# Kernel tuning notes

Measured on AMD Instinct MI355X. Metric: run time of the kernel, lower is better.

## Reference

```python
import jax, jax.numpy as jnp
import numpy as np

B, T, I, H, NL, O = 256, 512, 64, 256, 2, 4


def _lstm_layer(x, Wih, Whh, bih, bhh):
    # x: [B, T, I_in]; Wih: [4H, I_in]; Whh: [4H, H]; biases: [4H]
    # PyTorch gate order: i, f, g, o
    xg = jnp.einsum('bti,gi->btg', x, Wih) + (bih + bhh)  # [B, T, 4H]
    h0 = jnp.zeros((x.shape[0], Whh.shape[1]), x.dtype)
    c0 = jnp.zeros_like(h0)

    def step(carry, xg_t):
        h, c = carry
        g = xg_t + h @ Whh.T
        i, f, gg, o = jnp.split(g, 4, axis=-1)
        c = jax.nn.sigmoid(f) * c + jax.nn.sigmoid(i) * jnp.tanh(gg)
        h = jax.nn.sigmoid(o) * jnp.tanh(c)
        return (h, c), h

    (_, _), hs = jax.lax.scan(step, (h0, c0), jnp.swapaxes(xg, 0, 1))  # [T, B, H]
    return jnp.swapaxes(hs, 0, 1)  # [B, T, H]


def setup_inputs() -> dict:
    key = jax.random.key(0)
    ks = jax.random.split(key, 16)
    s = 1.0 / np.sqrt(H)
    u = lambda k, shape: jax.random.uniform(k, shape, jnp.float32, -s, s)
    return {
        'x': jax.random.normal(ks[0], (B, T, I), jnp.float32),
        'Wih0': u(ks[1], (4 * H, I)),
        'Whh0': u(ks[2], (4 * H, H)),
        'bih0': u(ks[3], (4 * H,)),
        'bhh0': u(ks[4], (4 * H,)),
        'Wih1': u(ks[5], (4 * H, H)),
        'Whh1': u(ks[6], (4 * H, H)),
        'bih1': u(ks[7], (4 * H,)),
        'bhh1': u(ks[8], (4 * H,)),
        'W1': u(ks[9], (5 * H, H)),
        'b1': u(ks[10], (5 * H,)),
        'W2': u(ks[11], (O, 5 * H)),
        'b2': u(ks[12], (O,)),
    }


def reference(x, Wih0, Whh0, bih0, bhh0, Wih1, Whh1, bih1, bhh1, W1, b1, W2, b2):
    h1 = _lstm_layer(x, Wih0, Whh0, bih0, bhh0)   # [B, T, H]
    h2 = _lstm_layer(h1, Wih1, Whh1, bih1, bhh1)  # [B, T, H]
    last = h2[:, -1, :]                            # [B, H]
    y = last @ W1.T + b1                           # [B, 5H]
    y = y @ W2.T + b2                              # [B, O]
    return y
```

## Files before the change

kernel.cpp:

```cpp
#include <hip/hip_runtime.h>
#include <stdint.h>

typedef unsigned short u16;
typedef unsigned int   u32;
typedef unsigned long long u64;
typedef __bf16 bf16_t;
typedef bf16_t bf16x8 __attribute__((ext_vector_type(8)));
typedef float  f32x4  __attribute__((ext_vector_type(4)));
typedef int    i32x4  __attribute__((ext_vector_type(4)));

#define NSTEPS 512
#define SPIN_LIM  (1<<17)
#define RETRY_LIM (1<<13)

#define WS_RING1 0u
#define WS_RING2 1048576u
#define WS_PROG  2097152u
#define WS_TOTAL 2098176u

#define SMEM_BYTES (64*520*2)

__device__ __forceinline__ u16 f2bf(float f) {
  u32 u = __float_as_uint(f);
  return (u16)((u + 0x7fffu + ((u >> 16) & 1u)) >> 16);
}
__device__ __forceinline__ float bf2f(u16 b) { return __uint_as_float(((u32)b) << 16); }
__device__ __forceinline__ float sigf(float x) { return 1.f / (1.f + __expf(-x)); }
__device__ __forceinline__ float tanhf_(float x) {
  float e = __expf(-2.f * fabsf(x));
  float t = (1.f - e) / (1.f + e);
  return x >= 0.f ? t : -t;
}

__device__ __forceinline__ void pub_u32(u32* p, u32 v) {
  (void)__hip_atomic_exchange(p, v, __ATOMIC_RELAXED, __HIP_MEMORY_SCOPE_AGENT);
}
__device__ __forceinline__ u64 ld_u64_sc1(const u64* p) {
  u64 v; asm volatile("global_load_dwordx2 %0, %1, off sc1\n\ts_waitcnt vmcnt(0)"
                      : "=v"(v) : "v"(p) : "memory"); return v;
}

#define LD16_W(A, P)                                                       \
  asm volatile(                                                            \
    "global_load_dwordx4 %0,  %16, off sc1\n\t"                            \
    "global_load_dwordx4 %1,  %16, off offset:16 sc1\n\t"                  \
    "global_load_dwordx4 %2,  %16, off offset:128 sc1\n\t"                 \
    "global_load_dwordx4 %3,  %16, off offset:144 sc1\n\t"                 \
    "global_load_dwordx4 %4,  %16, off offset:256 sc1\n\t"                 \
    "global_load_dwordx4 %5,  %16, off offset:272 sc1\n\t"                 \
    "global_load_dwordx4 %6,  %16, off offset:384 sc1\n\t"                 \
    "global_load_dwordx4 %7,  %16, off offset:400 sc1\n\t"                 \
    "global_load_dwordx4 %8,  %16, off offset:512 sc1\n\t"                 \
    "global_load_dwordx4 %9,  %16, off offset:528 sc1\n\t"                 \
    "global_load_dwordx4 %10, %16, off offset:640 sc1\n\t"                 \
    "global_load_dwordx4 %11, %16, off offset:656 sc1\n\t"                 \
    "global_load_dwordx4 %12, %16, off offset:768 sc1\n\t"                 \
    "global_load_dwordx4 %13, %16, off offset:784 sc1\n\t"                 \
    "global_load_dwordx4 %14, %16, off offset:896 sc1\n\t"                 \
    "global_load_dwordx4 %15, %16, off offset:912 sc1\n\t"                 \
    "s_waitcnt vmcnt(0)"                                                   \
    : "=&v"(A[0]), "=&v"(A[1]), "=&v"(A[2]),  "=&v"(A[3]),                 \
      "=&v"(A[4]), "=&v"(A[5]), "=&v"(A[6]),  "=&v"(A[7]),                 \
      "=&v"(A[8]), "=&v"(A[9]), "=&v"(A[10]), "=&v"(A[11]),                \
      "=&v"(A[12]),"=&v"(A[13]),"=&v"(A[14]), "=&v"(A[15])                 \
    : "v"(P) : "memory")

#define TAGCHK(A, TB, BAD) do {                                            \
    _Pragma("unroll")                                                      \
    for (int q_ = 0; q_ < 16; ++q_)                                        \
      BAD |= ((u32)A[q_][0] ^ TB) | ((u32)A[q_][1] ^ TB)                   \
           | ((u32)A[q_][2] ^ TB) | ((u32)A[q_][3] ^ TB);                  \
  } while (0)

#define TAGPOLL(A, hp, want) do {                                          \
    u32 tb = ((u32)(want)) << 16; int it_ = 0;                             \
    for (;;) {                                                             \
      LD16_W(A, hp);                                                       \
      u32 bad = 0; TAGCHK(A, tb, bad); bad &= 0xffff0000u;                 \
      if (__all(bad == 0)) break;                                          \
      if (++it_ > RETRY_LIM) break;                                        \
      __builtin_amdgcn_s_sleep(1);                                         \
    }                                                                      \
  } while (0)

__device__ __forceinline__ bf16x8 frag_from(i32x4 lo, i32x4 hi) {
  union { u32 w[4]; bf16x8 v; } u_;
  u_.w[0] = ((u32)lo[0] & 0xffffu) | ((u32)lo[1] << 16);
  u_.w[1] = ((u32)lo[2] & 0xffffu) | ((u32)lo[3] << 16);
  u_.w[2] = ((u32)hi[0] & 0xffffu) | ((u32)hi[1] << 16);
  u_.w[3] = ((u32)hi[2] & 0xffffu) | ((u32)hi[3] << 16);
  return u_.v;
}
__device__ __forceinline__ bf16x8 pack_bf8(float4 a, float4 b) {
  union { u32 w[4]; bf16x8 v; } u_;
  u_.w[0] = (u32)f2bf(a.x) | ((u32)f2bf(a.y) << 16);
  u_.w[1] = (u32)f2bf(a.z) | ((u32)f2bf(a.w) << 16);
  u_.w[2] = (u32)f2bf(b.x) | ((u32)f2bf(b.y) << 16);
  u_.w[3] = (u32)f2bf(b.z) | ((u32)f2bf(b.w) << 16);
  return u_.v;
}

__device__ __forceinline__ void spin64(const int* f, int lane, int target) {
  if (target <= 0) return;
  int it = 0;
  for (;;) {
    int v = __hip_atomic_load(&f[lane], __ATOMIC_RELAXED, __HIP_MEMORY_SCOPE_AGENT);
    if (__all(v >= target)) return;
    if (++it > SPIN_LIM) return;
    __builtin_amdgcn_s_sleep(2);
  }
}

__global__ void ws_init_kernel(int* p, int n) {
  int i = blockIdx.x * blockDim.x + threadIdx.x;
  if (i < n)
    __hip_atomic_store(&p[i], 0, __ATOMIC_RELAXED, __HIP_MEMORY_SCOPE_AGENT);
}

__global__ void __launch_bounds__(256)
lstm_persistent(const float* __restrict__ x,
                const float* __restrict__ Wih0, const float* __restrict__ Whh0,
                const float* __restrict__ bih0, const float* __restrict__ bhh0,
                const float* __restrict__ Wih1, const float* __restrict__ Whh1,
                const float* __restrict__ bih1, const float* __restrict__ bhh1,
                const float* __restrict__ W1, const float* __restrict__ b1,
                const float* __restrict__ W2, const float* __restrict__ b2,
                float* __restrict__ out, char* __restrict__ ws)
{
  extern __shared__ u16 smem[];
  const int tid  = threadIdx.x;
  const int lane = tid & 63;
  const int wv   = tid >> 6;
  const int n16  = lane & 15;
  const int quad = lane >> 4;
  const int blk  = blockIdx.x;
  const int layer = blk >> 6;
  const int b    = blk & 63;
  const int bi   = b >> 4, j = b & 15;
  const int j16  = j * 16;
  const int rowg0 = bi * 64;
  const int widx = j*4 + wv;
  const int arow = wv*16 + n16;

  u32* r1g = (u32*)(ws + WS_RING1) + (size_t)bi * 4 * 16384;
  u32* r2g = (u32*)(ws + WS_RING2) + (size_t)bi * 4 * 16384;
  int* prg = (int*)(ws + WS_PROG) + bi * 64;

  float bg[4];
  #pragma unroll
  for (int nt = 0; nt < 4; ++nt) {
    int wrow = nt*256 + j16 + n16;
    bg[nt] = layer ? (bih1[wrow] + bhh1[wrow]) : (bih0[wrow] + bhh0[wrow]);
  }
  float cst[4] = {0.f,0.f,0.f,0.f};
  i32x4 h[16];

  if (layer == 0) {
    for (int i = 0; i < 20; ++i) {
      int u = tid + i*256;
      int lr = u / 80, c4 = u % 80;
      int wrow = (lr >> 4)*256 + j16 + (lr & 15);
      float4 v = (c4 < 16) ? *(const float4*)(Wih0 + (size_t)wrow*64 + c4*4)
                           : *(const float4*)(Whh0 + (size_t)wrow*256 + (c4-16)*4);
      u16* d = smem + lr*328 + c4*4;
      d[0]=f2bf(v.x); d[1]=f2bf(v.y); d[2]=f2bf(v.z); d[3]=f2bf(v.w);
    }
    __syncthreads();
    const u16* bP = smem + n16*328 + quad*8;

    for (int t = 0; t < NSTEPS; ++t) {
      const float* xp = x + ((size_t)(rowg0 + arow)*NSTEPS + t)*64 + quad*8;
      float4 xa = *(const float4*)(xp);
      float4 xb = *(const float4*)(xp + 4);
      float4 xc = *(const float4*)(xp + 32);
      float4 xd = *(const float4*)(xp + 36);
      if ((t & 1) == 0)
        spin64(prg, lane, t - 2);
      { const char* hp = (const char*)(r1g + ((t+3)&3)*16384) + arow*1024 + quad*32;
        TAGPOLL(h, hp, t); }
      bf16x8 a0 = pack_bf8(xa, xb), a1 = pack_bf8(xc, xd);
      f32x4 acc[4] = {{0,0,0,0},{0,0,0,0},{0,0,0,0},{0,0,0,0}};
      #pragma unroll
      for (int nt = 0; nt < 4; ++nt)
        acc[nt] = __builtin_amdgcn_mfma_f32_16x16x32_bf16(
            a0, *(const bf16x8*)(bP + nt*16*328), acc[nt], 0,0,0);
      #pragma unroll
      for (int nt = 0; nt < 4; ++nt)
        acc[nt] = __builtin_amdgcn_mfma_f32_16x16x32_bf16(
            a1, *(const bf16x8*)(bP + nt*16*328 + 32), acc[nt], 0,0,0);
      #pragma unroll
      for (int kc = 0; kc < 8; ++kc) {
        bf16x8 a = frag_from(h[2*kc], h[2*kc+1]);
        #pragma unroll
        for (int nt = 0; nt < 4; ++nt)
          acc[nt] = __builtin_amdgcn_mfma_f32_16x16x32_bf16(
              a, *(const bf16x8*)(bP + nt*16*328 + 64 + kc*32), acc[nt], 0,0,0);
      }
      u32 tag = ((u32)(t+1)) << 16;
      u32* dst = r1g + (t&3)*16384;
      #pragma unroll
      for (int r = 0; r < 4; ++r) {
        float gi = acc[0][r] + bg[0];
        float gf = acc[1][r] + bg[1];
        float gg = acc[2][r] + bg[2];
        float go = acc[3][r] + bg[3];
        float c  = sigf(gf)*cst[r] + sigf(gi)*tanhf_(gg);
        cst[r] = c;
        int rl = wv*16 + quad*4 + r;
        pub_u32(dst + rl*256 + j16 + n16, tag | (u32)f2bf(sigf(go)*tanhf_(c)));
      }
    }
    return;
  }

  for (int i = 0; i < 32; ++i) {
    int u = tid + i*256;
    int lr = u >> 7, c4 = u & 127;
    int wrow = (lr >> 4)*256 + j16 + (lr & 15);
    float4 v = (c4 < 64) ? *(const float4*)(Wih1 + (size_t)wrow*256 + c4*4)
                         : *(const float4*)(Whh1 + (size_t)wrow*256 + (c4-64)*4);
    u16* d = smem + lr*520 + c4*4;
    d[0]=f2bf(v.x); d[1]=f2bf(v.y); d[2]=f2bf(v.z); d[3]=f2bf(v.w);
  }
  __syncthreads();
  const u16* bP = smem + n16*520 + quad*8;
  i32x4 g[16];

  for (int t = 0; t < NSTEPS; ++t) {
    { const char* hp = (const char*)(r1g + (t&3)*16384) + arow*1024 + quad*32;
      TAGPOLL(h, hp, t+1); }
    if (lane == 0)
      __hip_atomic_store(&prg[widx], t+1, __ATOMIC_RELAXED, __HIP_MEMORY_SCOPE_AGENT);
    f32x4 acc[4] = {{0,0,0,0},{0,0,0,0},{0,0,0,0},{0,0,0,0}};
    #pragma unroll
    for (int kc = 0; kc < 8; ++kc) {
      bf16x8 a = frag_from(h[2*kc], h[2*kc+1]);
      #pragma unroll
      for (int nt = 0; nt < 4; ++nt)
        acc[nt] = __builtin_amdgcn_mfma_f32_16x16x32_bf16(
            a, *(const bf16x8*)(bP + nt*16*520 + kc*32), acc[nt], 0,0,0);
    }
    { const char* hp = (const char*)(r2g + ((t+3)&3)*16384) + arow*1024 + quad*32;
      TAGPOLL(g, hp, t); }
    #pragma unroll
    for (int kc = 0; kc < 8; ++kc) {
      bf16x8 a = frag_from(g[2*kc], g[2*kc+1]);
      #pragma unroll
      for (int nt = 0; nt < 4; ++nt)
        acc[nt] = __builtin_amdgcn_mfma_f32_16x16x32_bf16(
            a, *(const bf16x8*)(bP + nt*16*520 + 256 + kc*32), acc[nt], 0,0,0);
    }
    u32 tag = ((u32)(t+1)) << 16;
    u32* dst = r2g + (t&3)*16384;
    #pragma unroll
    for (int r = 0; r < 4; ++r) {
      float gi = acc[0][r] + bg[0];
      float gf = acc[1][r] + bg[1];
      float gg = acc[2][r] + bg[2];
      float go = acc[3][r] + bg[3];
      float c  = sigf(gf)*cst[r] + sigf(gi)*tanhf_(gg);
      cst[r] = c;
      int rl = wv*16 + quad*4 + r;
      pub_u32(dst + rl*256 + j16 + n16, tag | (u32)f2bf(sigf(go)*tanhf_(c)));
    }
  }

  {
    float* lastsh = (float*)smem;
    float* y1sh   = lastsh + 1024;
    float* psum   = y1sh + 5120;
    __syncthreads();
    {
      int row = tid >> 6, c = tid & 63;
      int lr = (b & 15)*4 + row;
      #pragma unroll
      for (int rep = 0; rep < 2; ++rep) {
        int cc = c + rep*64;
        const u64* p = (const u64*)((const char*)(r2g + 3*16384) + lr*1024 + cc*8);
        u64 v = 0; int it = 0;
        for (;;) {
          v = ld_u64_sc1(p);
          if (((v >> 16) & 0xffffull) == 512 && (v >> 48) == 512) break;
          if (++it > RETRY_LIM) break;
          __builtin_amdgcn_s_sleep(1);
        }
        lastsh[row*256 + cc*2 + 0] = bf2f((u16)(v & 0xffffu));
        lastsh[row*256 + cc*2 + 1] = bf2f((u16)((v >> 32) & 0xffffu));
      }
    }
    __syncthreads();
    for (int i = 0; i < 5; ++i) {
      int m = tid + i*256;
      const float* wr = W1 + (size_t)m*256;
      float a0=0.f,a1=0.f,a2=0.f,a3=0.f;
      for (int k = 0; k < 256; ++k) {
        float w = wr[k];
        a0 += w*lastsh[k];     a1 += w*lastsh[256+k];
        a2 += w*lastsh[512+k]; a3 += w*lastsh[768+k];
      }
      float bb = b1[m];
      y1sh[m] = a0+bb; y1sh[1280+m] = a1+bb; y1sh[2560+m] = a2+bb; y1sh[3840+m] = a3+bb;
    }
    __syncthreads();
    if (tid < 64) {
      int row = tid >> 4, o = (tid >> 2) & 3, q = tid & 3;
      const float* w2r = W2 + (size_t)o*1280 + q*320;
      const float* yr  = y1sh + row*1280 + q*320;
      float s = 0.f;
      for (int m = 0; m < 320; ++m) s += w2r[m]*yr[m];
      psum[tid] = s;
    }
    __syncthreads();
    if (tid < 16) {
      int row = tid >> 2, o = tid & 3;
      out[(b*4 + row)*4 + o] = b2[o] + psum[tid*4+0] + psum[tid*4+1]
                                     + psum[tid*4+2] + psum[tid*4+3];
    }
  }
}

extern "C" void kernel_launch(void* const* d_in, const int* in_sizes, int n_in,
                              void* d_out, int out_size, void* d_ws, size_t ws_size,
                              hipStream_t stream) {
  (void)in_sizes; (void)n_in; (void)out_size; (void)ws_size;
  const float* x    = (const float*)d_in[0];
  const float* Wih0 = (const float*)d_in[1];
  const float* Whh0 = (const float*)d_in[2];
  const float* bih0 = (const float*)d_in[3];
  const float* bhh0 = (const float*)d_in[4];
  const float* Wih1 = (const float*)d_in[5];
  const float* Whh1 = (const float*)d_in[6];
  const float* bih1 = (const float*)d_in[7];
  const float* bhh1 = (const float*)d_in[8];
  const float* W1   = (const float*)d_in[9];
  const float* b1   = (const float*)d_in[10];
  const float* W2   = (const float*)d_in[11];
  const float* b2   = (const float*)d_in[12];
  float* out = (float*)d_out;
  char* ws   = (char*)d_ws;

  hipLaunchKernelGGL(ws_init_kernel, dim3((WS_TOTAL/4 + 255)/256), dim3(256),
                     0, stream, (int*)ws, (int)(WS_TOTAL/4));

  hipFuncSetAttribute((const void*)lstm_persistent,
                      hipFuncAttributeMaxDynamicSharedMemorySize, SMEM_BYTES);

  void* args[] = { (void*)&x, (void*)&Wih0, (void*)&Whh0, (void*)&bih0, (void*)&bhh0,
                   (void*)&Wih1, (void*)&Whh1, (void*)&bih1, (void*)&bhh1,
                   (void*)&W1, (void*)&b1, (void*)&W2, (void*)&b2,
                   (void*)&out, (void*)&ws };
  hipLaunchCooperativeKernel((const void*)lstm_persistent, dim3(128), dim3(256),
                             args, SMEM_BYTES, stream);
}
```

Measured before the change: 2.766 ms.

## Fold four batch groups into each workgroup and launch 32 blocks

Each workgroup now loops over all four batch groups inside every timestep instead of owning one, so the grid shrinks from 128 to 32 cooperative blocks. Each block keeps four cell-state sets and reuses its staged weight slice across the groups. The FC head is widened so each block handles 16 rows. The intent is fewer blocks taking part in the cross-block flag polling and some interleaving of the four groups' dependency chains. The cost is four times the serial work per block per step, on far fewer compute units.

```diff
diff --git a/kernel.cpp b/kernel.cpp
--- a/kernel.cpp
+++ b/kernel.cpp
@@ -18,7 +18,7 @@
 #define WS_PROG  2097152u
 #define WS_TOTAL 2098176u
 
-#define SMEM_BYTES (64*520*2)
+#define SMEM_BYTES 99328
 
 __device__ __forceinline__ u16 f2bf(float f) {
   u32 u = __float_as_uint(f);
@@ -134,17 +134,15 @@
   const int n16  = lane & 15;
   const int quad = lane >> 4;
   const int blk  = blockIdx.x;
-  const int layer = blk >> 6;
-  const int b    = blk & 63;
-  const int bi   = b >> 4, j = b & 15;
+  const int layer = blk >> 4;
+  const int j    = blk & 15;
   const int j16  = j * 16;
-  const int rowg0 = bi * 64;
   const int widx = j*4 + wv;
   const int arow = wv*16 + n16;
 
-  u32* r1g = (u32*)(ws + WS_RING1) + (size_t)bi * 4 * 16384;
-  u32* r2g = (u32*)(ws + WS_RING2) + (size_t)bi * 4 * 16384;
-  int* prg = (int*)(ws + WS_PROG) + bi * 64;
+  u32* ring1 = (u32*)(ws + WS_RING1);
+  u32* ring2 = (u32*)(ws + WS_RING2);
+  int* prog  = (int*)(ws + WS_PROG);
 
   float bg[4];
   #pragma unroll
@@ -152,7 +150,11 @@
     int wrow = nt*256 + j16 + n16;
     bg[nt] = layer ? (bih1[wrow] + bhh1[wrow]) : (bih0[wrow] + bhh0[wrow]);
   }
-  float cst[4] = {0.f,0.f,0.f,0.f};
+  float cst[4][4];
+  #pragma unroll
+  for (int bi = 0; bi < 4; ++bi)
+    #pragma unroll
+    for (int r = 0; r < 4; ++r) cst[bi][r] = 0.f;
   i32x4 h[16];
 
   if (layer == 0) {
@@ -169,45 +171,50 @@
     const u16* bP = smem + n16*328 + quad*8;
 
     for (int t = 0; t < NSTEPS; ++t) {
-      const float* xp = x + ((size_t)(rowg0 + arow)*NSTEPS + t)*64 + quad*8;
-      float4 xa = *(const float4*)(xp);
-      float4 xb = *(const float4*)(xp + 4);
-      float4 xc = *(const float4*)(xp + 32);
-      float4 xd = *(const float4*)(xp + 36);
-      if ((t & 1) == 0)
-        spin64(prg, lane, t - 2);
-      { const char* hp = (const char*)(r1g + ((t+3)&3)*16384) + arow*1024 + quad*32;
-        TAGPOLL(h, hp, t); }
-      bf16x8 a0 = pack_bf8(xa, xb), a1 = pack_bf8(xc, xd);
-      f32x4 acc[4] = {{0,0,0,0},{0,0,0,0},{0,0,0,0},{0,0,0,0}};
-      #pragma unroll
-      for (int nt = 0; nt < 4; ++nt)
-        acc[nt] = __builtin_amdgcn_mfma_f32_16x16x32_bf16(
-            a0, *(const bf16x8*)(bP + nt*16*328), acc[nt], 0,0,0);
-      #pragma unroll
-      for (int nt = 0; nt < 4; ++nt)
-        acc[nt] = __builtin_amdgcn_mfma_f32_16x16x32_bf16(
-            a1, *(const bf16x8*)(bP + nt*16*328 + 32), acc[nt], 0,0,0);
-      #pragma unroll
-      for (int kc = 0; kc < 8; ++kc) {
-        bf16x8 a = frag_from(h[2*kc], h[2*kc+1]);
+      #pragma unroll
+      for (int bi = 0; bi < 4; ++bi) {
+        u32* r1g = ring1 + (size_t)bi * 65536;
+        int* prg = prog + bi * 64;
+        const float* xp = x + ((size_t)(bi*64 + arow)*NSTEPS + t)*64 + quad*8;
+        float4 xa = *(const float4*)(xp);
+        float4 xb = *(const float4*)(xp + 4);
+        float4 xc = *(const float4*)(xp + 32);
+        float4 xd = *(const float4*)(xp + 36);
+        if ((t & 1) == 0)
+          spin64(prg, lane, t - 2);
+        { const char* hp = (const char*)(r1g + ((t+3)&3)*16384) + arow*1024 + quad*32;
+          TAGPOLL(h, hp, t); }
+        bf16x8 a0 = pack_bf8(xa, xb), a1 = pack_bf8(xc, xd);
+        f32x4 acc[4] = {{0,0,0,0},{0,0,0,0},{0,0,0,0},{0,0,0,0}};
         #pragma unroll
         for (int nt = 0; nt < 4; ++nt)
           acc[nt] = __builtin_amdgcn_mfma_f32_16x16x32_bf16(
-              a, *(const bf16x8*)(bP + nt*16*328 + 64 + kc*32), acc[nt], 0,0,0);
-      }
-      u32 tag = ((u32)(t+1)) << 16;
-      u32* dst = r1g + (t&3)*16384;
-      #pragma unroll
-      for (int r = 0; r < 4; ++r) {
-        float gi = acc[0][r] + bg[0];
-        float gf = acc[1][r] + bg[1];
-        float gg = acc[2][r] + bg[2];
-        float go = acc[3][r] + bg[3];
-        float c  = sigf(gf)*cst[r] + sigf(gi)*tanhf_(gg);
-        cst[r] = c;
-        int rl = wv*16 + quad*4 + r;
-        pub_u32(dst + rl*256 + j16 + n16, tag | (u32)f2bf(sigf(go)*tanhf_(c)));
+              a0, *(const bf16x8*)(bP + nt*16*328), acc[nt], 0,0,0);
+        #pragma unroll
+        for (int nt = 0; nt < 4; ++nt)
+          acc[nt] = __builtin_amdgcn_mfma_f32_16x16x32_bf16(
+              a1, *(const bf16x8*)(bP + nt*16*328 + 32), acc[nt], 0,0,0);
+        #pragma unroll
+        for (int kc = 0; kc < 8; ++kc) {
+          bf16x8 a = frag_from(h[2*kc], h[2*kc+1]);
+          #pragma unroll
+          for (int nt = 0; nt < 4; ++nt)
+            acc[nt] = __builtin_amdgcn_mfma_f32_16x16x32_bf16(
+                a, *(const bf16x8*)(bP + nt*16*328 + 64 + kc*32), acc[nt], 0,0,0);
+        }
+        u32 tag = ((u32)(t+1)) << 16;
+        u32* dst = r1g + (t&3)*16384;
+        #pragma unroll
+        for (int r = 0; r < 4; ++r) {
+          float gi = acc[0][r] + bg[0];
+          float gf = acc[1][r] + bg[1];
+          float gg = acc[2][r] + bg[2];
+          float go = acc[3][r] + bg[3];
+          float c  = sigf(gf)*cst[bi][r] + sigf(gi)*tanhf_(gg);
+          cst[bi][r] = c;
+          int rl = wv*16 + quad*4 + r;
+          pub_u32(dst + rl*256 + j16 + n16, tag | (u32)f2bf(sigf(go)*tanhf_(c)));
+        }
       }
     }
     return;
@@ -227,56 +234,63 @@
   i32x4 g[16];
 
   for (int t = 0; t < NSTEPS; ++t) {
-    { const char* hp = (const char*)(r1g + (t&3)*16384) + arow*1024 + quad*32;
-      TAGPOLL(h, hp, t+1); }
-    if (lane == 0)
-      __hip_atomic_store(&prg[widx], t+1, __ATOMIC_RELAXED, __HIP_MEMORY_SCOPE_AGENT);
-    f32x4 acc[4] = {{0,0,0,0},{0,0,0,0},{0,0,0,0},{0,0,0,0}};
     #pragma unroll
-    for (int kc = 0; kc < 8; ++kc) {
-      bf16x8 a = frag_from(h[2*kc], h[2*kc+1]);
-      #pragma unroll
-      for (int nt = 0; nt < 4; ++nt)
-        acc[nt] = __builtin_amdgcn_mfma_f32_16x16x32_bf16(
-            a, *(const bf16x8*)(bP + nt*16*520 + kc*32), acc[nt], 0,0,0);
-    }
-    { const char* hp = (const char*)(r2g + ((t+3)&3)*16384) + arow*1024 + quad*32;
-      TAGPOLL(g, hp, t); }
-    #pragma unroll
-    for (int kc = 0; kc < 8; ++kc) {
-      bf16x8 a = frag_from(g[2*kc], g[2*kc+1]);
-      #pragma unroll
-      for (int nt = 0; nt < 4; ++nt)
-        acc[nt] = __builtin_amdgcn_mfma_f32_16x16x32_bf16(
-            a, *(const bf16x8*)(bP + nt*16*520 + 256 + kc*32), acc[nt], 0,0,0);
-    }
-    u32 tag = ((u32)(t+1)) << 16;
-    u32* dst = r2g + (t&3)*16384;
-    #pragma unroll
-    for (int r = 0; r < 4; ++r) {
-      float gi = acc[0][r] + bg[0];
-      float gf = acc[1][r] + bg[1];
-      float gg = acc[2][r] + bg[2];
-      float go = acc[3][r] + bg[3];
-      float c  = sigf(gf)*cst[r] + sigf(gi)*tanhf_(gg);
-      cst[r] = c;
-      int rl = wv*16 + quad*4 + r;
-      pub_u32(dst + rl*256 + j16 + n16, tag | (u32)f2bf(sigf(go)*tanhf_(c)));
+    for (int bi = 0; bi < 4; ++bi) {
+      u32* r1g = ring1 + (size_t)bi * 65536;
+      u32* r2g = ring2 + (size_t)bi * 65536;
+      int* prg = prog + bi * 64;
+      { const char* hp = (const char*)(r1g + (t&3)*16384) + arow*1024 + quad*32;
+        TAGPOLL(h, hp, t+1); }
+      if (lane == 0)
+        __hip_atomic_store(&prg[widx], t+1, __ATOMIC_RELAXED, __HIP_MEMORY_SCOPE_AGENT);
+      f32x4 acc[4] = {{0,0,0,0},{0,0,0,0},{0,0,0,0},{0,0,0,0}};
+      #pragma unroll
+      for (int kc = 0; kc < 8; ++kc) {
+        bf16x8 a = frag_from(h[2*kc], h[2*kc+1]);
+        #pragma unroll
+        for (int nt = 0; nt < 4; ++nt)
+          acc[nt] = __builtin_amdgcn_mfma_f32_16x16x32_bf16(
+              a, *(const bf16x8*)(bP + nt*16*520 + kc*32), acc[nt], 0,0,0);
+      }
+      { const char* hp = (const char*)(r2g + ((t+3)&3)*16384) + arow*1024 + quad*32;
+        TAGPOLL(g, hp, t); }
+      #pragma unroll
+      for (int kc = 0; kc < 8; ++kc) {
+        bf16x8 a = frag_from(g[2*kc], g[2*kc+1]);
+        #pragma unroll
+        for (int nt = 0; nt < 4; ++nt)
+          acc[nt] = __builtin_amdgcn_mfma_f32_16x16x32_bf16(
+              a, *(const bf16x8*)(bP + nt*16*520 + 256 + kc*32), acc[nt], 0,0,0);
+      }
+      u32 tag = ((u32)(t+1)) << 16;
+      u32* dst = r2g + (t&3)*16384;
+      #pragma unroll
+      for (int r = 0; r < 4; ++r) {
+        float gi = acc[0][r] + bg[0];
+        float gf = acc[1][r] + bg[1];
+        float gg = acc[2][r] + bg[2];
+        float go = acc[3][r] + bg[3];
+        float c  = sigf(gf)*cst[bi][r] + sigf(gi)*tanhf_(gg);
+        cst[bi][r] = c;
+        int rl = wv*16 + quad*4 + r;
+        pub_u32(dst + rl*256 + j16 + n16, tag | (u32)f2bf(sigf(go)*tanhf_(c)));
+      }
     }
   }
 
   {
     float* lastsh = (float*)smem;
-    float* y1sh   = lastsh + 1024;
-    float* psum   = y1sh + 5120;
-    __syncthreads();
+    float* y1sh   = lastsh + 4096;
+    float* psum   = y1sh + 20480;
+    __syncthreads();
+    const u32* r2e = ring2 + (size_t)(j >> 2) * 65536 + 3*16384;
     {
-      int row = tid >> 6, c = tid & 63;
-      int lr = (b & 15)*4 + row;
-      #pragma unroll
-      for (int rep = 0; rep < 2; ++rep) {
-        int cc = c + rep*64;
-        const u64* p = (const u64*)((const char*)(r2g + 3*16384) + lr*1024 + cc*8);
+      int row = tid >> 4, c16 = tid & 15;
+      int lr = (j & 3)*16 + row;
+      #pragma unroll
+      for (int k = 0; k < 8; ++k) {
+        int cc = c16*8 + k;
+        const u64* p = (const u64*)((const char*)r2e + lr*1024 + cc*8);
         u64 v = 0; int it = 0;
         for (;;) {
           v = ld_u64_sc1(p);
@@ -291,18 +305,24 @@
     __syncthreads();
     for (int i = 0; i < 5; ++i) {
       int m = tid + i*256;
-      const float* wr = W1 + (size_t)m*256;
-      float a0=0.f,a1=0.f,a2=0.f,a3=0.f;
-      for (int k = 0; k < 256; ++k) {
-        float w = wr[k];
-        a0 += w*lastsh[k];     a1 += w*lastsh[256+k];
-        a2 += w*lastsh[512+k]; a3 += w*lastsh[768+k];
+      const float4* wr4 = (const float4*)(W1 + (size_t)m*256);
+      float a[16];
+      #pragma unroll
+      for (int jj = 0; jj < 16; ++jj) a[jj] = 0.f;
+      for (int k4 = 0; k4 < 64; ++k4) {
+        float4 w4 = wr4[k4];
+        #pragma unroll
+        for (int jj = 0; jj < 16; ++jj) {
+          const float* ls = lastsh + jj*256 + k4*4;
+          a[jj] += w4.x*ls[0] + w4.y*ls[1] + w4.z*ls[2] + w4.w*ls[3];
+        }
       }
       float bb = b1[m];
-      y1sh[m] = a0+bb; y1sh[1280+m] = a1+bb; y1sh[2560+m] = a2+bb; y1sh[3840+m] = a3+bb;
-    }
-    __syncthreads();
-    if (tid < 64) {
+      #pragma unroll
+      for (int jj = 0; jj < 16; ++jj) y1sh[jj*1280 + m] = a[jj] + bb;
+    }
+    __syncthreads();
+    {
       int row = tid >> 4, o = (tid >> 2) & 3, q = tid & 3;
       const float* w2r = W2 + (size_t)o*1280 + q*320;
       const float* yr  = y1sh + row*1280 + q*320;
@@ -311,10 +331,12 @@
       psum[tid] = s;
     }
     __syncthreads();
-    if (tid < 16) {
+    if (tid < 64) {
       int row = tid >> 2, o = tid & 3;
-      out[(b*4 + row)*4 + o] = b2[o] + psum[tid*4+0] + psum[tid*4+1]
-                                     + psum[tid*4+2] + psum[tid*4+3];
+      out[(j*16 + row)*4 + o] = b2[o] + psum[row*16 + o*4 + 0]
+                                      + psum[row*16 + o*4 + 1]
+                                      + psum[row*16 + o*4 + 2]
+                                      + psum[row*16 + o*4 + 3];
     }
   }
 }
@@ -349,6 +371,6 @@
                    (void*)&Wih1, (void*)&Whh1, (void*)&bih1, (void*)&bhh1,
                    (void*)&W1, (void*)&b1, (void*)&W2, (void*)&b2,
                    (void*)&out, (void*)&ws };
-  hipLaunchCooperativeKernel((const void*)lstm_persistent, dim3(128), dim3(256),
+  hipLaunchCooperativeKernel((const void*)lstm_persistent, dim3(32), dim3(256),
                              args, SMEM_BYTES, stream);
 }
```

Result: slower. 9.226 ms (+233.5%).

## Give each layer-0 LSTM block twice the hidden columns, shrinking the grid

Applied to the files above, without the earlier changes.

Layer 0 now runs on 32 blocks instead of 64. Each block owns 32 hidden units per batch group, held as two 16-column halves with doubled MFMA tiles, bias registers and cell-state registers. Layer 1 keeps its 64-block split, and the cooperative grid drops from 128 to 96 blocks. The aim is fewer producer blocks per batch group and less cross-block traffic on the step-to-step handoff. The cost is double the matrix-multiply work per layer-0 wave on the serial recurrence, plus twice the weight footprint in shared memory.

```diff
diff --git a/kernel.cpp b/kernel.cpp
--- a/kernel.cpp
+++ b/kernel.cpp
@@ -18,7 +18,7 @@
 #define WS_PROG  2097152u
 #define WS_TOTAL 2098176u
 
-#define SMEM_BYTES (64*520*2)
+#define SMEM_BYTES (128*328*2)
 
 __device__ __forceinline__ u16 f2bf(float f) {
   u32 u = __float_as_uint(f);
@@ -134,32 +134,32 @@
   const int n16  = lane & 15;
   const int quad = lane >> 4;
   const int blk  = blockIdx.x;
-  const int layer = blk >> 6;
-  const int b    = blk & 63;
-  const int bi   = b >> 4, j = b & 15;
-  const int j16  = j * 16;
-  const int rowg0 = bi * 64;
-  const int widx = j*4 + wv;
+  const int layer = (blk < 32) ? 0 : 1;
   const int arow = wv*16 + n16;
-
-  u32* r1g = (u32*)(ws + WS_RING1) + (size_t)bi * 4 * 16384;
-  u32* r2g = (u32*)(ws + WS_RING2) + (size_t)bi * 4 * 16384;
-  int* prg = (int*)(ws + WS_PROG) + bi * 64;
-
-  float bg[4];
-  #pragma unroll
-  for (int nt = 0; nt < 4; ++nt) {
-    int wrow = nt*256 + j16 + n16;
-    bg[nt] = layer ? (bih1[wrow] + bhh1[wrow]) : (bih0[wrow] + bhh0[wrow]);
-  }
-  float cst[4] = {0.f,0.f,0.f,0.f};
   i32x4 h[16];
 
   if (layer == 0) {
-    for (int i = 0; i < 20; ++i) {
+    const int b   = blk;
+    const int bi  = b >> 3, j = b & 7;
+    const int j32 = j * 32;
+    const int rowg0 = bi * 64;
+    u32* r1g = (u32*)(ws + WS_RING1) + (size_t)bi * 4 * 16384;
+    int* prg = (int*)(ws + WS_PROG) + bi * 64;
+
+    float bg[4][2];
+    #pragma unroll
+    for (int g4 = 0; g4 < 4; ++g4)
+      #pragma unroll
+      for (int hf = 0; hf < 2; ++hf) {
+        int wrow = g4*256 + j32 + hf*16 + n16;
+        bg[g4][hf] = bih0[wrow] + bhh0[wrow];
+      }
+    float cst[2][4] = {{0.f,0.f,0.f,0.f},{0.f,0.f,0.f,0.f}};
+
+    for (int i = 0; i < 40; ++i) {
       int u = tid + i*256;
       int lr = u / 80, c4 = u % 80;
-      int wrow = (lr >> 4)*256 + j16 + (lr & 15);
+      int wrow = (lr >> 5)*256 + j32 + (lr & 31);
       float4 v = (c4 < 16) ? *(const float4*)(Wih0 + (size_t)wrow*64 + c4*4)
                            : *(const float4*)(Whh0 + (size_t)wrow*256 + (c4-16)*4);
       u16* d = smem + lr*328 + c4*4;
@@ -179,39 +179,59 @@
       { const char* hp = (const char*)(r1g + ((t+3)&3)*16384) + arow*1024 + quad*32;
         TAGPOLL(h, hp, t); }
       bf16x8 a0 = pack_bf8(xa, xb), a1 = pack_bf8(xc, xd);
-      f32x4 acc[4] = {{0,0,0,0},{0,0,0,0},{0,0,0,0},{0,0,0,0}};
-      #pragma unroll
-      for (int nt = 0; nt < 4; ++nt)
+      f32x4 acc[8];
+      #pragma unroll
+      for (int nt = 0; nt < 8; ++nt) acc[nt] = (f32x4){0.f,0.f,0.f,0.f};
+      #pragma unroll
+      for (int nt = 0; nt < 8; ++nt)
         acc[nt] = __builtin_amdgcn_mfma_f32_16x16x32_bf16(
             a0, *(const bf16x8*)(bP + nt*16*328), acc[nt], 0,0,0);
       #pragma unroll
-      for (int nt = 0; nt < 4; ++nt)
+      for (int nt = 0; nt < 8; ++nt)
         acc[nt] = __builtin_amdgcn_mfma_f32_16x16x32_bf16(
             a1, *(const bf16x8*)(bP + nt*16*328 + 32), acc[nt], 0,0,0);
       #pragma unroll
       for (int kc = 0; kc < 8; ++kc) {
         bf16x8 a = frag_from(h[2*kc], h[2*kc+1]);
         #pragma unroll
-        for (int nt = 0; nt < 4; ++nt)
+        for (int nt = 0; nt < 8; ++nt)
           acc[nt] = __builtin_amdgcn_mfma_f32_16x16x32_bf16(
               a, *(const bf16x8*)(bP + nt*16*328 + 64 + kc*32), acc[nt], 0,0,0);
       }
       u32 tag = ((u32)(t+1)) << 16;
       u32* dst = r1g + (t&3)*16384;
       #pragma unroll
-      for (int r = 0; r < 4; ++r) {
-        float gi = acc[0][r] + bg[0];
-        float gf = acc[1][r] + bg[1];
-        float gg = acc[2][r] + bg[2];
-        float go = acc[3][r] + bg[3];
-        float c  = sigf(gf)*cst[r] + sigf(gi)*tanhf_(gg);
-        cst[r] = c;
-        int rl = wv*16 + quad*4 + r;
-        pub_u32(dst + rl*256 + j16 + n16, tag | (u32)f2bf(sigf(go)*tanhf_(c)));
-      }
+      for (int hf = 0; hf < 2; ++hf)
+        #pragma unroll
+        for (int r = 0; r < 4; ++r) {
+          float gi = acc[0+hf][r] + bg[0][hf];
+          float gf = acc[2+hf][r] + bg[1][hf];
+          float gg = acc[4+hf][r] + bg[2][hf];
+          float go = acc[6+hf][r] + bg[3][hf];
+          float c  = sigf(gf)*cst[hf][r] + sigf(gi)*tanhf_(gg);
+          cst[hf][r] = c;
+          int rl = wv*16 + quad*4 + r;
+          pub_u32(dst + rl*256 + j32 + hf*16 + n16, tag | (u32)f2bf(sigf(go)*tanhf_(c)));
+        }
     }
     return;
   }
+
+  const int b   = blk - 32;
+  const int bi  = b >> 4, j = b & 15;
+  const int j16 = j * 16;
+  const int widx = j*4 + wv;
+  u32* r1g = (u32*)(ws + WS_RING1) + (size_t)bi * 4 * 16384;
+  u32* r2g = (u32*)(ws + WS_RING2) + (size_t)bi * 4 * 16384;
+  int* prg = (int*)(ws + WS_PROG) + bi * 64;
+
+  float bg[4];
+  #pragma unroll
+  for (int nt = 0; nt < 4; ++nt) {
+    int wrow = nt*256 + j16 + n16;
+    bg[nt] = bih1[wrow] + bhh1[wrow];
+  }
+  float cst[4] = {0.f,0.f,0.f,0.f};
 
   for (int i = 0; i < 32; ++i) {
     int u = tid + i*256;
@@ -349,6 +369,6 @@
                    (void*)&Wih1, (void*)&Whh1, (void*)&bih1, (void*)&bhh1,
                    (void*)&W1, (void*)&b1, (void*)&W2, (void*)&b2,
                    (void*)&out, (void*)&ws };
-  hipLaunchCooperativeKernel((const void*)lstm_persistent, dim3(128), dim3(256),
+  hipLaunchCooperativeKernel((const void*)lstm_persistent, dim3(96), dim3(256),
                              args, SMEM_BYTES, stream);
 }
```

New measurement: 3.163 ms. +14.3%, slower.
